# Performance work log

Measured on AMD Instinct MI355X. Metric: run time of the kernel, lower is better.

Reference implementation:

```python
import jax, jax.numpy as jnp
import numpy as np

B, L, DIN, DM, NL, DI, DS, DC, DTR, NC = 32, 1024, 9, 512, 4, 1024, 16, 4, 32, 12


def setup_inputs() -> dict:
    key = jax.random.key(0)
    ks = jax.random.split(key, 8)
    s = 0.02
    return {
        'x': jax.random.normal(ks[0], (B, L, DIN), jnp.float32),
        'ip_w': jax.random.normal(ks[1], (DM, DIN), jnp.float32) * s,
        'ip_b': jnp.zeros((DM,), jnp.float32),
        'ln_g': jnp.ones((NL, DM), jnp.float32),
        'ln_b': jnp.zeros((NL, DM), jnp.float32),
        'in_proj_w': jax.random.normal(ks[2], (NL, 2 * DI, DM), jnp.float32) * s,
        'conv_w': jax.random.normal(ks[3], (NL, DI, DC), jnp.float32) * s,
        'conv_b': jnp.zeros((NL, DI), jnp.float32),
        'x_proj_w': jax.random.normal(ks[4], (NL, DTR + 2 * DS, DI), jnp.float32) * s,
        'dt_w': jax.random.normal(ks[5], (NL, DI, DTR), jnp.float32) * s,
        'dt_b': jnp.zeros((NL, DI), jnp.float32),
        'A_log': jnp.tile(jnp.log(jnp.arange(1, DS + 1, dtype=jnp.float32))[None, None, :], (NL, DI, 1)),
        'D': jnp.ones((NL, DI), jnp.float32),
        'out_proj_w': jax.random.normal(ks[6], (NL, DM, DI), jnp.float32) * s,
        'fc_w': jax.random.normal(ks[7], (NC, DM), jnp.float32) * s,
        'fc_b': jnp.zeros((NC,), jnp.float32),
    }


def _layernorm(x, g, b):
    m = jnp.mean(x, axis=-1, keepdims=True)
    v = jnp.var(x, axis=-1, keepdims=True)
    return (x - m) * jax.lax.rsqrt(v + 1e-5) * g + b


def _mamba(x, in_w, cw, cb, xp_w, dtw, dtb, Alog, Dp, ow):
    # x: (B, L, DM)
    xz = jnp.einsum('bld,ed->ble', x, in_w)          # (B, L, 2*DI)
    u, z = jnp.split(xz, 2, axis=-1)
    # causal depthwise conv1d over time
    ut = jnp.transpose(u, (0, 2, 1))                  # (B, DI, L)
    ut = jnp.pad(ut, ((0, 0), (0, 0), (DC - 1, 0)))
    conv = jax.lax.conv_general_dilated(
        ut, cw[:, None, :], (1,), 'VALID',
        feature_group_count=DI, dimension_numbers=('NCH', 'OIH', 'NCH'))
    u = jax.nn.silu(jnp.transpose(conv + cb[None, :, None], (0, 2, 1)))  # (B, L, DI)
    x_dbl = jnp.einsum('ble,fe->blf', u, xp_w)        # (B, L, DTR+2*DS)
    dt, Bm, Cm = jnp.split(x_dbl, [DTR, DTR + DS], axis=-1)
    delta = jax.nn.softplus(jnp.einsum('blr,er->ble', dt, dtw) + dtb)    # (B, L, DI)
    A = -jnp.exp(Alog)                                # (DI, DS)

    def step(h, inp):
        d_t, B_t, C_t, u_t = inp                      # (B,DI) (B,DS) (B,DS) (B,DI)
        dA = jnp.exp(d_t[:, :, None] * A)             # (B, DI, DS)
        h = dA * h + (d_t * u_t)[:, :, None] * B_t[:, None, :]
        y = jnp.einsum('bes,bs->be', h, C_t)
        return h, y

    xs = (jnp.moveaxis(delta, 1, 0), jnp.moveaxis(Bm, 1, 0),
          jnp.moveaxis(Cm, 1, 0), jnp.moveaxis(u, 1, 0))
    h0 = jnp.zeros((x.shape[0], DI, DS), x.dtype)
    _, ys = jax.lax.scan(step, h0, xs)                # (L, B, DI)
    y = jnp.moveaxis(ys, 0, 1) + u * Dp
    y = y * jax.nn.silu(z)
    return jnp.einsum('ble,de->bld', y, ow)           # (B, L, DM)


def reference(x, ip_w, ip_b, ln_g, ln_b, in_proj_w, conv_w, conv_b, x_proj_w, dt_w, dt_b, A_log, D, out_proj_w, fc_w, fc_b):
    h = jnp.einsum('bli,di->bld', x, ip_w) + ip_b
    for i in range(NL):
        res = h
        hn = _layernorm(h, ln_g[i], ln_b[i])
        h = _mamba(hn, in_proj_w[i], conv_w[i], conv_b[i], x_proj_w[i],
                   dt_w[i], dt_b[i], A_log[i], D[i], out_proj_w[i]) + res
    pooled = jnp.mean(h, axis=1)                      # (B, DM); dropout is identity in eval
    return pooled @ fc_w.T + fc_b                     # (B, NC)
```

## Files before the change

kernel.cpp:

```cpp
#include <hip/hip_runtime.h>
#include <hip/hip_bf16.h>

#define B_   32
#define L_   1024
#define DIN_ 9
#define DM_  512
#define NL_  4
#define DI_  1024
#define DS_  16
#define DC_  4
#define DTR_ 32
#define NC_  12
#define M_   (B_*L_)
#define NCC_ 2
#define MC_  (M_/NCC_)
#define BC_  (B_/NCC_)
#define NCH_ 16
#define CHT_ 64

typedef unsigned short u16;
typedef __attribute__((ext_vector_type(8))) short bf16x8;
typedef __attribute__((ext_vector_type(4))) float f32x4;

__device__ __forceinline__ float bf2f(u16 h){
  union { unsigned int u; float f; } v; v.u = ((unsigned int)h) << 16; return v.f;
}
__device__ __forceinline__ u16 f2bf(float f){
  union { float f; unsigned int u; } v; v.f = f;
  unsigned int u = v.u;
  return (u16)((u + 0x7fffu + ((u >> 16) & 1u)) >> 16);
}
__device__ __forceinline__ float siluf(float x){
  return x * __builtin_amdgcn_rcpf(1.f + __expf(-x));
}

__device__ __forceinline__ void gload_lds16(const u16* g, u16* l){
  __builtin_amdgcn_global_load_lds(
      (const __attribute__((address_space(1))) void*)(unsigned long long)(const void*)g,
      (__attribute__((address_space(3))) void*)(unsigned int)(unsigned long long)(void*)l,
      16, 0, 0);
}

#define NW1_ (NL_*2*DI_*DM_)
#define NW3_ (NL_*DM_*DI_)
#define NW2_ (NL_*64*DI_)
#define NW4_ (NL_*DI_*DTR_)
__global__ __launch_bounds__(256) void cast4_kernel(const float* __restrict__ a,
                                                    const float* __restrict__ c,
                                                    const float* __restrict__ e,
                                                    const float* __restrict__ f,
                                                    u16* __restrict__ oa,
                                                    u16* __restrict__ oc,
                                                    u16* __restrict__ oe,
                                                    u16* __restrict__ of){
  int i = blockIdx.x * 256 + threadIdx.x;
  if (i < NW1_) oa[i] = f2bf(a[i]);
  else if (i < NW1_ + NW3_) oc[i - NW1_] = f2bf(c[i - NW1_]);
  else if (i < NW1_ + NW3_ + NW2_) oe[i - NW1_ - NW3_] = f2bf(e[i - NW1_ - NW3_]);
  else if (i < NW1_ + NW3_ + NW2_ + NW4_)
    of[i - NW1_ - NW3_ - NW2_] = f2bf(f[i - NW1_ - NW3_ - NW2_]);
}

__global__ __launch_bounds__(256) void prep_kernel(const float* __restrict__ convw,
                                                   const float* __restrict__ A_log,
                                                   float* __restrict__ cwt,
                                                   float* __restrict__ At){
  int gid = blockIdx.x * 256 + threadIdx.x;
  int l = gid >> 10, e = gid & (DI_ - 1);
  float4 cw = *(const float4*)(convw + (size_t)gid * 4);
  cwt[(l * 4 + 0) * DI_ + e] = cw.x;
  cwt[(l * 4 + 1) * DI_ + e] = cw.y;
  cwt[(l * 4 + 2) * DI_ + e] = cw.z;
  cwt[(l * 4 + 3) * DI_ + e] = cw.w;
  const float* ar = A_log + (size_t)gid * DS_;
#pragma unroll
  for (int s = 0; s < DS_; s++)
    At[((size_t)l * DS_ + s) * DI_ + e] = -__expf(ar[s]);
}

__global__ __launch_bounds__(512) void inproj_kernel(const float* __restrict__ x,
                                                     const float* __restrict__ w,
                                                     const float* __restrict__ bias,
                                                     u16* __restrict__ h){
  int m = blockIdx.x;
  int d = threadIdx.x;
  __shared__ float xr[DIN_];
  if (threadIdx.x < DIN_) xr[threadIdx.x] = x[(size_t)m * DIN_ + threadIdx.x];
  __syncthreads();
  float a = bias[d];
#pragma unroll
  for (int i = 0; i < DIN_; i++) a += xr[i] * w[d * DIN_ + i];
  h[(size_t)m * DM_ + d] = f2bf(a);
}

__global__ __launch_bounds__(256) void ln_kernel(const u16* __restrict__ h,
                                                 const float* __restrict__ g,
                                                 const float* __restrict__ bt,
                                                 u16* __restrict__ hn){
  int row = blockIdx.x * 4 + (threadIdx.x >> 6);
  int lane = threadIdx.x & 63;
  const u16* hr = h + (size_t)row * DM_ + lane * 8;
  ushort4 a0 = *(const ushort4*)(hr);
  ushort4 a1 = *(const ushort4*)(hr + 4);
  float v[8];
  v[0]=bf2f(a0.x); v[1]=bf2f(a0.y); v[2]=bf2f(a0.z); v[3]=bf2f(a0.w);
  v[4]=bf2f(a1.x); v[5]=bf2f(a1.y); v[6]=bf2f(a1.z); v[7]=bf2f(a1.w);
  float s = 0.f, q = 0.f;
#pragma unroll
  for (int i = 0; i < 8; i++){ s += v[i]; q += v[i]*v[i]; }
#pragma unroll
  for (int o = 32; o; o >>= 1){ s += __shfl_xor(s, o); q += __shfl_xor(q, o); }
  float mean = s * (1.f / DM_);
  float rstd = rsqrtf(q * (1.f / DM_) - mean * mean + 1e-5f);
  float4 g0 = *(const float4*)(g + lane * 8);
  float4 g1 = *(const float4*)(g + lane * 8 + 4);
  float4 b0 = *(const float4*)(bt + lane * 8);
  float4 b1 = *(const float4*)(bt + lane * 8 + 4);
  ushort4 o0, o1;
  o0.x = f2bf((v[0]-mean)*rstd*g0.x + b0.x);
  o0.y = f2bf((v[1]-mean)*rstd*g0.y + b0.y);
  o0.z = f2bf((v[2]-mean)*rstd*g0.z + b0.z);
  o0.w = f2bf((v[3]-mean)*rstd*g0.w + b0.w);
  o1.x = f2bf((v[4]-mean)*rstd*g1.x + b1.x);
  o1.y = f2bf((v[5]-mean)*rstd*g1.y + b1.y);
  o1.z = f2bf((v[6]-mean)*rstd*g1.z + b1.z);
  o1.w = f2bf((v[7]-mean)*rstd*g1.w + b1.w);
  u16* op = hn + (size_t)row * DM_ + lane * 8;
  *(ushort4*)(op)     = o0;
  *(ushort4*)(op + 4) = o1;
}

__global__ __launch_bounds__(256) void conv8_kernel(const u16* __restrict__ xu,
                                                    const float* __restrict__ cwt,
                                                    const float* __restrict__ cbp,
                                                    u16* __restrict__ ub){
  int idx = blockIdx.x * 256 + threadIdx.x;
  int e8 = (idx & 127) * 8;
  int bl = idx >> 7;
  int l = bl & (L_ - 1);
  const u16* p = xu + (size_t)bl * DI_ + e8;
  float acc[8];
  {
    float4 c0 = *(const float4*)(cbp + e8);
    float4 c1 = *(const float4*)(cbp + e8 + 4);
    acc[0]=c0.x; acc[1]=c0.y; acc[2]=c0.z; acc[3]=c0.w;
    acc[4]=c1.x; acc[5]=c1.y; acc[6]=c1.z; acc[7]=c1.w;
  }
#pragma unroll
  for (int d = 0; d < 4; d++){
    if (l - 3 + d >= 0){
      const u16* q = p - (size_t)(3 - d) * DI_;
      ushort4 v0 = *(const ushort4*)q, v1 = *(const ushort4*)(q + 4);
      float4 w0 = *(const float4*)(cwt + d * DI_ + e8);
      float4 w1 = *(const float4*)(cwt + d * DI_ + e8 + 4);
      acc[0] += bf2f(v0.x) * w0.x; acc[1] += bf2f(v0.y) * w0.y;
      acc[2] += bf2f(v0.z) * w0.z; acc[3] += bf2f(v0.w) * w0.w;
      acc[4] += bf2f(v1.x) * w1.x; acc[5] += bf2f(v1.y) * w1.y;
      acc[6] += bf2f(v1.z) * w1.z; acc[7] += bf2f(v1.w) * w1.w;
    }
  }
  ushort4 h0, h1;
  h0.x = f2bf(siluf(acc[0])); h0.y = f2bf(siluf(acc[1]));
  h0.z = f2bf(siluf(acc[2])); h0.w = f2bf(siluf(acc[3]));
  h1.x = f2bf(siluf(acc[4])); h1.y = f2bf(siluf(acc[5]));
  h1.z = f2bf(siluf(acc[6])); h1.w = f2bf(siluf(acc[7]));
  u16* o = ub + (size_t)bl * DI_ + e8;
  *(ushort4*)o = h0;
  *(ushort4*)(o + 4) = h1;
}

template<int BM, int BN, int BK, int EPI, int TPB>
__global__ __launch_bounds__(TPB)
void gemm_bt(const u16* __restrict__ A, int lda,
             const u16* __restrict__ Bw,
             u16* Cb, u16* Cb2, const u16* Res,
             const float* __restrict__ bias,
             int N, int K, int nsplit, int gx){
  constexpr int CH = BK / 8;
  constexpr int MASK = CH - 1;
  constexpr int WROWS = TPB / 128;
  constexpr int WM = BM / WROWS, WN = BN / 2;
  constexpr int FM = WM / 16, FN = WN / 16;
  __shared__ u16 As_[BM * BK];
  __shared__ u16 Bs_[BN * BK];
  const int tid = threadIdx.x;
  const int lane = tid & 63;
  const int wid = tid >> 6;
  const int wr = wid >> 1, wc = wid & 1;
  int bm, bn;
  {
    const int wg = blockIdx.x;
    const int gy = (int)gridDim.x / gx;
    const int ypx = gy >> 3;
    const int xcd = wg & 7;
    const int idx = wg >> 3;
    const int y = xcd * ypx + (idx % ypx);
    const int x = idx / ypx;
    bm = y * BM; bn = x * BN;
  }
  f32x4 acc[FM][FN];
#pragma unroll
  for (int i = 0; i < FM; i++)
#pragma unroll
    for (int j = 0; j < FN; j++) acc[i][j] = f32x4{0.f, 0.f, 0.f, 0.f};
  constexpr int LA = BM * BK / (TPB * 8);
  constexpr int LB = BN * BK / (TPB * 8);
  const int wbase = wid * 64;
  for (int k0 = 0; k0 < K; k0 += BK){
    __syncthreads();
#pragma unroll
    for (int i = 0; i < LA; i++){
      int chunk = i * TPB + tid;
      int row = chunk / CH, cs = chunk & MASK;
      int cg = cs ^ (row & MASK);
      const u16* g = A + (size_t)(bm + row) * lda + k0 + cg * 8;
      gload_lds16(g, &As_[(i * TPB + wbase) * 8]);
    }
#pragma unroll
    for (int i = 0; i < LB; i++){
      int chunk = i * TPB + tid;
      int row = chunk / CH, cs = chunk & MASK;
      int cg = cs ^ (row & MASK);
      const u16* g = Bw + (size_t)(bn + row) * K + k0 + cg * 8;
      gload_lds16(g, &Bs_[(i * TPB + wbase) * 8]);
    }
    __syncthreads();
#pragma unroll
    for (int kk = 0; kk < BK / 32; kk++){
      bf16x8 af[FM], bfr[FN];
      const int kch = kk * 4 + (lane >> 4);
#pragma unroll
      for (int mi = 0; mi < FM; mi++){
        int r = wr * WM + mi * 16 + (lane & 15);
        af[mi] = *(const bf16x8*)(&As_[r * BK + ((kch ^ (r & MASK))) * 8]);
      }
#pragma unroll
      for (int ni = 0; ni < FN; ni++){
        int r = wc * WN + ni * 16 + (lane & 15);
        bfr[ni] = *(const bf16x8*)(&Bs_[r * BK + ((kch ^ (r & MASK))) * 8]);
      }
#pragma unroll
      for (int mi = 0; mi < FM; mi++)
#pragma unroll
        for (int ni = 0; ni < FN; ni++)
          acc[mi][ni] = __builtin_amdgcn_mfma_f32_16x16x32_bf16(af[mi], bfr[ni], acc[mi][ni], 0, 0, 0);
    }
  }
  const int rq = (lane >> 4) * 4, cl = lane & 15;
#pragma unroll
  for (int mi = 0; mi < FM; mi++){
#pragma unroll
    for (int ni = 0; ni < FN; ni++){
      const int n = bn + wc * WN + ni * 16 + cl;
#pragma unroll
      for (int j = 0; j < 4; j++){
        const int m = bm + wr * WM + mi * 16 + rq + j;
        float v = acc[mi][ni][j];
        if constexpr (EPI == 0){
          Cb[(size_t)m * N + n] = f2bf(v);
        } else if constexpr (EPI == 1){
          float xx = v + bias[n];
          float sp = (xx > 20.f) ? xx : __logf(1.f + __expf(xx));
          Cb[(size_t)m * N + n] = f2bf(sp);
        } else if constexpr (EPI == 2){
          const size_t off = (size_t)m * N + n;
          Cb[off] = f2bf(v + bf2f(Res[off]));
        } else {
          if (n < nsplit){
            Cb[(size_t)m * nsplit + n] = f2bf(v);
          } else {
            Cb2[(size_t)m * nsplit + (n - nsplit)] = f2bf(siluf(v));
          }
        }
      }
    }
  }
}

__global__ __launch_bounds__(256)
void scan1_kernel(const u16* __restrict__ ub, const u16* __restrict__ dlt,
                  const u16* __restrict__ xdb,
                  const float* __restrict__ At, float* __restrict__ sb){
  const int tid = threadIdx.x;
  const int e = blockIdx.x * 256 + tid;
  const int c = blockIdx.y, b = blockIdx.z;
  __shared__ float Bsh[CHT_][DS_];
  {
    int row = tid >> 2, col4 = (tid & 3) * 4;
    const u16* p = xdb + ((size_t)b * L_ + (size_t)c * CHT_ + row) * 64 + 32 + col4;
    ushort4 v = *(const ushort4*)p;
    Bsh[row][col4+0] = bf2f(v.x); Bsh[row][col4+1] = bf2f(v.y);
    Bsh[row][col4+2] = bf2f(v.z); Bsh[row][col4+3] = bf2f(v.w);
  }
  __syncthreads();
  float As[DS_];
  bool fast = true;
#pragma unroll
  for (int s = 0; s < DS_; s++){
    As[s] = At[(size_t)s * DI_ + e];
    fast = fast && (fabsf(As[s] + (float)(s + 1)) <= 1e-3f * (s + 1));
  }
  float h[DS_];
#pragma unroll
  for (int s = 0; s < DS_; s++) h[s] = 0.f;
  float sdd = 0.f;
  const size_t base = ((size_t)b * L_ + (size_t)c * CHT_) * DI_ + e;
  if (fast){
    for (int t = 0; t < CHT_; t++){
      const size_t idx = base + (size_t)t * DI_;
      float ut = bf2f(ub[idx]);
      float delta = bf2f(dlt[idx]);
      sdd += delta;
      float du = delta * ut;
      float e1 = __expf(-delta);
      float e2 = e1*e1, e4 = e2*e2, e8 = e4*e4;
      float dA[DS_] = {e1, e2, e2*e1, e4, e4*e1, e4*e2, e4*e2*e1, e8,
                       e8*e1, e8*e2, e8*e2*e1, e8*e4, e8*e4*e1, e8*e4*e2,
                       e8*e4*e2*e1, e8*e8};
      const float* r = &Bsh[t][0];
#pragma unroll
      for (int s = 0; s < DS_; s++)
        h[s] = fmaf(dA[s], h[s], du * r[s]);
    }
  } else {
    for (int t = 0; t < CHT_; t++){
      const size_t idx = base + (size_t)t * DI_;
      float ut = bf2f(ub[idx]);
      float delta = bf2f(dlt[idx]);
      sdd += delta;
      float du = delta * ut;
      const float* r = &Bsh[t][0];
#pragma unroll
      for (int s = 0; s < DS_; s++)
        h[s] = fmaf(__expf(delta * As[s]), h[s], du * r[s]);
    }
  }
  float* p = sb + ((size_t)c * (BC_ * DI_) + (size_t)b * DI_ + e) * 32;
  if (fast){
    float e1 = __expf(-sdd);
    float e2 = e1*e1, e4 = e2*e2, e8 = e4*e4;
    float ap[DS_] = {e1, e2, e2*e1, e4, e4*e1, e4*e2, e4*e2*e1, e8,
                     e8*e1, e8*e2, e8*e2*e1, e8*e4, e8*e4*e1, e8*e4*e2,
                     e8*e4*e2*e1, e8*e8};
#pragma unroll
    for (int s = 0; s < DS_; s++) p[s] = ap[s];
  } else {
#pragma unroll
    for (int s = 0; s < DS_; s++) p[s] = __expf(As[s] * sdd);
  }
#pragma unroll
  for (int s = 0; s < DS_; s++) p[16 + s] = h[s];
}

__global__ __launch_bounds__(256)
void scan2_kernel(float* __restrict__ sb){
  const int be = blockIdx.x * 256 + threadIdx.x;
  const int BE = BC_ * DI_;
  float h[DS_];
#pragma unroll
  for (int s = 0; s < DS_; s++) h[s] = 0.f;
  for (int c = 0; c < NCH_; c++){
    float* p = sb + ((size_t)c * BE + be) * 32;
    float4 a0 = *(const float4*)(p);
    float4 a1 = *(const float4*)(p + 4);
    float4 a2 = *(const float4*)(p + 8);
    float4 a3 = *(const float4*)(p + 12);
    float4 h0 = *(const float4*)(p + 16);
    float4 h1 = *(const float4*)(p + 20);
    float4 h2 = *(const float4*)(p + 24);
    float4 h3 = *(const float4*)(p + 28);
    float av[16] = {a0.x,a0.y,a0.z,a0.w, a1.x,a1.y,a1.z,a1.w,
                    a2.x,a2.y,a2.z,a2.w, a3.x,a3.y,a3.z,a3.w};
    float hv[16] = {h0.x,h0.y,h0.z,h0.w, h1.x,h1.y,h1.z,h1.w,
                    h2.x,h2.y,h2.z,h2.w, h3.x,h3.y,h3.z,h3.w};
    float4 w0, w1, w2, w3;
    float* wv[4] = {&w0.x, &w1.x, &w2.x, &w3.x};
#pragma unroll
    for (int s = 0; s < DS_; s++){
      float hi = h[s];
      h[s] = av[s] * hi + hv[s];
      wv[s >> 2][s & 3] = hi;
    }
    *(float4*)(p + 16) = w0;
    *(float4*)(p + 20) = w1;
    *(float4*)(p + 24) = w2;
    *(float4*)(p + 28) = w3;
  }
}

__global__ __launch_bounds__(256)
void scan3_kernel(const u16* __restrict__ ub, const u16* __restrict__ dlt,
                  u16* __restrict__ zy, const u16* __restrict__ xdb,
                  const float* __restrict__ At, const float* __restrict__ Dp,
                  const float* __restrict__ sb){
  const int tid = threadIdx.x;
  const int e = blockIdx.x * 256 + tid;
  const int c = blockIdx.y, b = blockIdx.z;
  __shared__ float BC[CHT_][32];
  {
#pragma unroll
    for (int q = 0; q < 2; q++){
      int idx = q * 256 + tid;
      int row = idx >> 3, col4 = (idx & 7) * 4;
      const u16* p = xdb + ((size_t)b * L_ + (size_t)c * CHT_ + row) * 64 + 32 + col4;
      ushort4 v = *(const ushort4*)p;
      BC[row][col4+0] = bf2f(v.x); BC[row][col4+1] = bf2f(v.y);
      BC[row][col4+2] = bf2f(v.z); BC[row][col4+3] = bf2f(v.w);
    }
  }
  __syncthreads();
  float As[DS_];
  bool fast = true;
#pragma unroll
  for (int s = 0; s < DS_; s++){
    As[s] = At[(size_t)s * DI_ + e];
    fast = fast && (fabsf(As[s] + (float)(s + 1)) <= 1e-3f * (s + 1));
  }
  const float Dv = Dp[e];
  const float* ip = sb + ((size_t)c * (BC_ * DI_) + (size_t)b * DI_ + e) * 32 + 16;
  float h[DS_];
#pragma unroll
  for (int s = 0; s < DS_; s++) h[s] = ip[s];
  const size_t base = ((size_t)b * L_ + (size_t)c * CHT_) * DI_ + e;
  if (fast){
    for (int t = 0; t < CHT_; t++){
      const size_t idx = base + (size_t)t * DI_;
      float ut = bf2f(ub[idx]);
      float delta = bf2f(dlt[idx]);
      float du = delta * ut;
      float e1 = __expf(-delta);
      float e2 = e1*e1, e4 = e2*e2, e8 = e4*e4;
      float dA[DS_] = {e1, e2, e2*e1, e4, e4*e1, e4*e2, e4*e2*e1, e8,
                       e8*e1, e8*e2, e8*e2*e1, e8*e4, e8*e4*e1, e8*e4*e2,
                       e8*e4*e2*e1, e8*e8};
      const float* r = &BC[t][0];
      float yv = 0.f;
#pragma unroll
      for (int s = 0; s < DS_; s++){
        h[s] = fmaf(dA[s], h[s], du * r[s]);
        yv = fmaf(h[s], r[16 + s], yv);
      }
      float zs = bf2f(zy[idx]);
      zy[idx] = f2bf((yv + ut * Dv) * zs);
    }
  } else {
    for (int t = 0; t < CHT_; t++){
      const size_t idx = base + (size_t)t * DI_;
      float ut = bf2f(ub[idx]);
      float delta = bf2f(dlt[idx]);
      float du = delta * ut;
      const float* r = &BC[t][0];
      float yv = 0.f;
#pragma unroll
      for (int s = 0; s < DS_; s++){
        h[s] = fmaf(__expf(delta * As[s]), h[s], du * r[s]);
        yv = fmaf(h[s], r[16 + s], yv);
      }
      float zs = bf2f(zy[idx]);
      zy[idx] = f2bf((yv + ut * Dv) * zs);
    }
  }
}

__global__ __launch_bounds__(256) void pool_kernel(const u16* __restrict__ h,
                                                   float* __restrict__ part){
  int d = blockIdx.x * 256 + threadIdx.x;
  int b = blockIdx.y;
  int p = blockIdx.z;
  float s = 0.f;
  const u16* hp = h + ((size_t)b * L_ + p * 128) * DM_ + d;
  for (int l = 0; l < 128; l++) s += bf2f(hp[(size_t)l * DM_]);
  part[((size_t)p * B_ + b) * DM_ + d] = s;
}

__global__ __launch_bounds__(256) void fc_kernel(const float* __restrict__ part,
                                                 const float* __restrict__ fcw,
                                                 const float* __restrict__ fcb,
                                                 float* __restrict__ out){
  int b = blockIdx.x;
  int tid = threadIdx.x;
  __shared__ float pd[DM_];
  for (int d = tid; d < DM_; d += 256){
    float s = 0.f;
    for (int p = 0; p < 8; p++) s += part[((size_t)p * B_ + b) * DM_ + d];
    pd[d] = s * (1.f / L_);
  }
  __syncthreads();
  int wid = tid >> 6, lane = tid & 63;
  for (int c = wid; c < NC_; c += 4){
    float s = 0.f;
    for (int d = lane; d < DM_; d += 64) s += pd[d] * fcw[c * DM_ + d];
#pragma unroll
    for (int o = 32; o; o >>= 1) s += __shfl_xor(s, o);
    if (lane == 0) out[b * NC_ + c] = s + fcb[c];
  }
}

extern "C" void kernel_launch(void* const* d_in, const int* in_sizes, int n_in,
                              void* d_out, int out_size, void* d_ws, size_t ws_size,
                              hipStream_t stream){
  const float* x     = (const float*)d_in[0];
  const float* ip_w  = (const float*)d_in[1];
  const float* ip_b  = (const float*)d_in[2];
  const float* ln_g  = (const float*)d_in[3];
  const float* ln_b  = (const float*)d_in[4];
  const float* inpw  = (const float*)d_in[5];
  const float* convw = (const float*)d_in[6];
  const float* convb = (const float*)d_in[7];
  const float* xpw   = (const float*)d_in[8];
  const float* dtw   = (const float*)d_in[9];
  const float* dtb   = (const float*)d_in[10];
  const float* Alog  = (const float*)d_in[11];
  const float* Dp    = (const float*)d_in[12];
  const float* outw  = (const float*)d_in[13];
  const float* fcw   = (const float*)d_in[14];
  const float* fcb   = (const float*)d_in[15];
  float* out = (float*)d_out;

  char* ws = (char*)d_ws;
  size_t off = 0;
  auto alloc = [&](size_t bytes) -> void* {
    void* p = ws + off; off += (bytes + 255) & ~(size_t)255; return p;
  };
  u16*    h16   = (u16*)   alloc((size_t)M_ * DM_ * 2);
  float*  part  = (float*) alloc((size_t)8 * B_ * DM_ * 4);
  u16*    w_in  = (u16*)   alloc((size_t)NW1_ * 2);
  u16*    w_out = (u16*)   alloc((size_t)NW3_ * 2);
  u16*    w_xp  = (u16*)   alloc((size_t)NW2_ * 2);
  u16*    w_dt  = (u16*)   alloc((size_t)NW4_ * 2);
  float*  cwt   = (float*) alloc((size_t)NL_ * 4 * DI_ * 4);
  float*  At    = (float*) alloc((size_t)NL_ * DS_ * DI_ * 4);
  u16*    xu    = (u16*)   alloc((size_t)MC_ * DI_ * 2);
  u16*    ub    = (u16*)   alloc((size_t)MC_ * DI_ * 2);
  u16*    xzs   = (u16*)   alloc((size_t)MC_ * DI_ * 2);
  u16*    dlt   = (u16*)   alloc((size_t)MC_ * DI_ * 2);
  u16*    xdb   = (u16*)   alloc((size_t)MC_ * 64 * 2);
  float*  sb    = (float*) alloc((size_t)NCH_ * BC_ * DI_ * 32 * 4);
  u16*    hn    = dlt;

  cast4_kernel<<<(NW1_ + NW3_ + NW2_ + NW4_ + 255) / 256, 256, 0, stream>>>(
      inpw, outw, xpw, dtw, w_in, w_out, w_xp, w_dt);
  prep_kernel<<<(NL_ * DI_) / 256, 256, 0, stream>>>(convw, Alog, cwt, At);
  inproj_kernel<<<M_, 512, 0, stream>>>(x, ip_w, ip_b, h16);

  const int GY  = MC_ / 128;
  const int GY2 = MC_ / 256;
  for (int i = 0; i < NL_; i++){
    for (int c = 0; c < NCC_; c++){
      u16* hc = h16 + (size_t)c * MC_ * DM_;

      ln_kernel<<<MC_ / 4, 256, 0, stream>>>(hc, ln_g + i * DM_, ln_b + i * DM_, hn);

      gemm_bt<256, 128, 64, 4, 512><<<16 * GY2, 512, 0, stream>>>(
          hn, DM_, w_in + (size_t)i * 2 * DI_ * DM_, xu, xzs, nullptr, nullptr,
          2 * DI_, DM_, DI_, 16);

      conv8_kernel<<<(MC_ * DI_ / 8) / 256, 256, 0, stream>>>(
          xu, cwt + (size_t)i * 4 * DI_, convb + i * DI_, ub);

      gemm_bt<128, 64, 64, 0, 256><<<1 * GY, 256, 0, stream>>>(
          ub, DI_, w_xp + (size_t)i * 64 * DI_, xdb, nullptr, nullptr, nullptr,
          64, DI_, 0, 1);

      gemm_bt<128, 128, 32, 1, 256><<<8 * GY, 256, 0, stream>>>(
          xdb, 64, w_dt + (size_t)i * DI_ * DTR_, dlt, nullptr, nullptr,
          dtb + i * DI_, DI_, DTR_, 0, 8);

      scan1_kernel<<<dim3(DI_ / 256, NCH_, BC_), 256, 0, stream>>>(
          ub, dlt, xdb, At + (size_t)i * DS_ * DI_, sb);
      scan2_kernel<<<(BC_ * DI_) / 256, 256, 0, stream>>>(sb);
      scan3_kernel<<<dim3(DI_ / 256, NCH_, BC_), 256, 0, stream>>>(
          ub, dlt, xzs, xdb, At + (size_t)i * DS_ * DI_, Dp + i * DI_, sb);

      gemm_bt<256, 128, 64, 2, 512><<<4 * GY2, 512, 0, stream>>>(
          xzs, DI_, w_out + (size_t)i * DM_ * DI_, hc, nullptr, hc,
          nullptr, DM_, DI_, 0, 4);
    }
  }

  pool_kernel<<<dim3(2, B_, 8), 256, 0, stream>>>(h16, part);
  fc_kernel<<<B_, 256, 0, stream>>>(part, fcw, fcb, out);
}
```

Baseline: 2.062 ms.

## Stage GEMM epilogue through shared memory and batch rows in input projection

The GEMM epilogue now writes accumulators to shared memory (reusing the A/B tile buffer) and then stores 16-byte vectors per thread, replacing scattered 2-byte global stores. Bias/softplus, residual add and SiLU are applied after an intermediate bf16 rounding. The input projection kernel processes 32 rows per block with weights held in registers and writes packed bf16 pairs. This reduces uncoalesced store traffic and per-row launch overhead, at the cost of extra barriers and slight extra rounding.

```diff
diff --git a/kernel.cpp b/kernel.cpp
--- a/kernel.cpp
+++ b/kernel.cpp
@@ -78,19 +78,35 @@
     At[((size_t)l * DS_ + s) * DI_ + e] = -__expf(ar[s]);
 }
 
-__global__ __launch_bounds__(512) void inproj_kernel(const float* __restrict__ x,
+__global__ __launch_bounds__(256) void inproj_kernel(const float* __restrict__ x,
                                                      const float* __restrict__ w,
                                                      const float* __restrict__ bias,
                                                      u16* __restrict__ h){
-  int m = blockIdx.x;
-  int d = threadIdx.x;
-  __shared__ float xr[DIN_];
-  if (threadIdx.x < DIN_) xr[threadIdx.x] = x[(size_t)m * DIN_ + threadIdx.x];
+  __shared__ float xs[32 * DIN_];
+  const int tid = threadIdx.x;
+  const int m0 = blockIdx.x * 32;
+  for (int i = tid; i < 32 * DIN_; i += 256) xs[i] = x[(size_t)m0 * DIN_ + i];
+  float w0[DIN_], w1[DIN_];
+  const int d0 = tid * 2;
+#pragma unroll
+  for (int i = 0; i < DIN_; i++){
+    w0[i] = w[(size_t)d0 * DIN_ + i];
+    w1[i] = w[(size_t)(d0 + 1) * DIN_ + i];
+  }
+  const float b0 = bias[d0], b1 = bias[d0 + 1];
   __syncthreads();
-  float a = bias[d];
-#pragma unroll
-  for (int i = 0; i < DIN_; i++) a += xr[i] * w[d * DIN_ + i];
-  h[(size_t)m * DM_ + d] = f2bf(a);
+  for (int r = 0; r < 32; r++){
+    float a0 = b0, a1 = b1;
+    const float* xr = &xs[r * DIN_];
+#pragma unroll
+    for (int i = 0; i < DIN_; i++){
+      float xv = xr[i];
+      a0 = fmaf(xv, w0[i], a0);
+      a1 = fmaf(xv, w1[i], a1);
+    }
+    unsigned int pk = ((unsigned int)f2bf(a1) << 16) | (unsigned int)f2bf(a0);
+    *(unsigned int*)(h + (size_t)(m0 + r) * DM_ + d0) = pk;
+  }
 }
 
 __global__ __launch_bounds__(256) void ln_kernel(const u16* __restrict__ h,
@@ -181,8 +197,13 @@
   constexpr int WROWS = TPB / 128;
   constexpr int WM = BM / WROWS, WN = BN / 2;
   constexpr int FM = WM / 16, FN = WN / 16;
-  __shared__ u16 As_[BM * BK];
-  __shared__ u16 Bs_[BN * BK];
+  constexpr int CROWS = (BM < 128) ? BM : 128;
+  constexpr int AB_U16 = BM * BK + BN * BK;
+  constexpr int CC_U16 = CROWS * BN;
+  constexpr int SM_U16 = (AB_U16 > CC_U16) ? AB_U16 : CC_U16;
+  __shared__ u16 smem[SM_U16];
+  u16* As_ = smem;
+  u16* Bs_ = smem + BM * BK;
   const int tid = threadIdx.x;
   const int lane = tid & 63;
   const int wid = tid >> 6;
@@ -247,30 +268,52 @@
     }
   }
   const int rq = (lane >> 4) * 4, cl = lane & 15;
-#pragma unroll
-  for (int mi = 0; mi < FM; mi++){
-#pragma unroll
-    for (int ni = 0; ni < FN; ni++){
-      const int n = bn + wc * WN + ni * 16 + cl;
-#pragma unroll
-      for (int j = 0; j < 4; j++){
-        const int m = bm + wr * WM + mi * 16 + rq + j;
-        float v = acc[mi][ni][j];
-        if constexpr (EPI == 0){
-          Cb[(size_t)m * N + n] = f2bf(v);
-        } else if constexpr (EPI == 1){
-          float xx = v + bias[n];
+  for (int r0 = 0; r0 < BM; r0 += CROWS){
+    __syncthreads();
+#pragma unroll
+    for (int mi = 0; mi < FM; mi++){
+      const int rowbase = wr * WM + mi * 16 + rq;
+      if (rowbase >= r0 && rowbase < r0 + CROWS){
+#pragma unroll
+        for (int ni = 0; ni < FN; ni++){
+          const int col = wc * WN + ni * 16 + cl;
+#pragma unroll
+          for (int j = 0; j < 4; j++)
+            smem[(rowbase + j - r0) * BN + col] = f2bf(acc[mi][ni][j]);
+        }
+      }
+    }
+    __syncthreads();
+    for (int idx = tid; idx < CROWS * (BN / 8); idx += TPB){
+      const int row = idx / (BN / 8);
+      const int c8  = idx - row * (BN / 8);
+      uint4 v = *(uint4*)&smem[row * BN + c8 * 8];
+      u16* pv = (u16*)&v;
+      const int m = bm + r0 + row;
+      const int nb = bn + c8 * 8;
+      if constexpr (EPI == 0){
+        *(uint4*)(Cb + (size_t)m * N + nb) = v;
+      } else if constexpr (EPI == 1){
+#pragma unroll
+        for (int j = 0; j < 8; j++){
+          float xx = bf2f(pv[j]) + bias[nb + j];
           float sp = (xx > 20.f) ? xx : __logf(1.f + __expf(xx));
-          Cb[(size_t)m * N + n] = f2bf(sp);
-        } else if constexpr (EPI == 2){
-          const size_t off = (size_t)m * N + n;
-          Cb[off] = f2bf(v + bf2f(Res[off]));
+          pv[j] = f2bf(sp);
+        }
+        *(uint4*)(Cb + (size_t)m * N + nb) = v;
+      } else if constexpr (EPI == 2){
+        uint4 rv = *(const uint4*)(Res + (size_t)m * N + nb);
+        const u16* pr = (const u16*)&rv;
+#pragma unroll
+        for (int j = 0; j < 8; j++) pv[j] = f2bf(bf2f(pv[j]) + bf2f(pr[j]));
+        *(uint4*)(Cb + (size_t)m * N + nb) = v;
+      } else {
+        if (nb < nsplit){
+          *(uint4*)(Cb + (size_t)m * nsplit + nb) = v;
         } else {
-          if (n < nsplit){
-            Cb[(size_t)m * nsplit + n] = f2bf(v);
-          } else {
-            Cb2[(size_t)m * nsplit + (n - nsplit)] = f2bf(siluf(v));
-          }
+#pragma unroll
+          for (int j = 0; j < 8; j++) pv[j] = f2bf(siluf(bf2f(pv[j])));
+          *(uint4*)(Cb2 + (size_t)m * nsplit + (nb - nsplit)) = v;
         }
       }
     }
@@ -541,7 +584,7 @@
   cast4_kernel<<<(NW1_ + NW3_ + NW2_ + NW4_ + 255) / 256, 256, 0, stream>>>(
       inpw, outw, xpw, dtw, w_in, w_out, w_xp, w_dt);
   prep_kernel<<<(NL_ * DI_) / 256, 256, 0, stream>>>(convw, Alog, cwt, At);
-  inproj_kernel<<<M_, 512, 0, stream>>>(x, ip_w, ip_b, h16);
+  inproj_kernel<<<M_ / 32, 256, 0, stream>>>(x, ip_w, ip_b, h16);
 
   const int GY  = MC_ / 128;
   const int GY2 = MC_ / 256;
```

After: 2.215 ms. 7.4% more time.
